# Performance work log

Hardware: AMD Instinct MI355X
Metric: run time of the kernel (lower is better)

The kernel has to match this reference:

```python
import jax, jax.numpy as jnp
import numpy as np

SPARSITY_RATIO = 0.1


def setup_inputs() -> dict:
    key = jax.random.key(0)
    ks = jax.random.split(key, 11)
    B, S, d = 4, 2048, 16  # d = n_sparse_dims + 2
    inp = {
        "full": jax.random.normal(ks[0], (B, S, d), dtype=jnp.float32),
        "sw1": jax.random.normal(ks[1], (d, 32), dtype=jnp.float32) * 0.1,
        "sb1": jax.random.normal(ks[2], (32,), dtype=jnp.float32) * 0.1,
        "sw2": jax.random.normal(ks[3], (32, 1), dtype=jnp.float32) * 0.1,
        "sb2": jax.random.normal(ks[4], (1,), dtype=jnp.float32) * 0.1,
        "mw1": jax.random.normal(ks[5], (3 * d, 64), dtype=jnp.float32) * 0.1,
        "mb1": jax.random.normal(ks[6], (64,), dtype=jnp.float32) * 0.1,
        "mw2": jax.random.normal(ks[7], (64, 32), dtype=jnp.float32) * 0.1,
        "mb2": jax.random.normal(ks[8], (32,), dtype=jnp.float32) * 0.1,
        "mw3": jax.random.normal(ks[9], (32, d), dtype=jnp.float32) * 0.1,
        "mb3": jax.random.normal(ks[10], (d,), dtype=jnp.float32) * 0.1,
    }
    return inp


def reference(full, sw1, sb1, sw2, sb2, mw1, mb1, mw2, mb2, mw3, mb3):
    B, S, d = full.shape
    k = max(1, int(S * SPARSITY_RATIO))  # static python int

    # importance scores: Linear(d,32) -> ReLU -> Linear(32,1)
    scores = (jax.nn.relu(full @ sw1 + sb1) @ sw2 + sb2)[..., 0]  # [B, S]
    _, top_idx = jax.lax.top_k(scores, k)  # [B, k]

    # gather selected tokens (keys == values)
    sel = jnp.take_along_axis(full, top_idx[:, :, None], axis=1)  # [B, k, d]

    # First MLP layer on concat([q, keys, values]) decomposed to avoid the
    # [B,S,k,3d] concat: mw1 splits into query / key / value blocks.
    w_q, w_k, w_v = mw1[:d], mw1[d:2 * d], mw1[2 * d:]
    q_part = full @ w_q                     # [B, S, 64]
    kv_part = sel @ (w_k + w_v)             # [B, k, 64]
    h1 = jax.nn.relu(q_part[:, :, None, :] + kv_part[:, None, :, :] + mb1)  # [B,S,k,64]
    h2 = jax.nn.relu(h1 @ mw2 + mb2)        # [B, S, k, 32]
    out = h2 @ mw3 + mb3                    # [B, S, k, d]
    return out.mean(axis=2)                 # [B, S, d]
```

## Files before the change

kernel.cpp:

```cpp
#include <hip/hip_runtime.h>
#include <hip/hip_bf16.h>

#define BB 4
#define SS 2048
#define DD 16
#define KK 204
#define JSPLIT 8

typedef __attribute__((ext_vector_type(8))) short short8;
typedef __attribute__((ext_vector_type(4))) float f32x4;

__device__ inline short f2bf(float x) {
  __hip_bfloat16 b = __float2bfloat16(x);
  return *reinterpret_cast<short*>(&b);
}

__global__ void __launch_bounds__(256) score_q_kernel(
    const float* __restrict__ full, const float* __restrict__ sw1,
    const float* __restrict__ sb1, const float* __restrict__ sw2,
    const float* __restrict__ sb2, const float* __restrict__ mw1,
    float* __restrict__ scores, float* __restrict__ qpart) {
  int idx = blockIdx.x * blockDim.x + threadIdx.x;
  if (idx >= BB * SS) return;
  float x[16];
  const float* xp = full + idx * DD;
#pragma unroll
  for (int i = 0; i < 16; i++) x[i] = xp[i];

  float sc = sb2[0];
#pragma unroll
  for (int n = 0; n < 32; n++) {
    float a = sb1[n];
#pragma unroll
    for (int k = 0; k < 16; k++) a += x[k] * sw1[k * 32 + n];
    a = fmaxf(a, 0.f);
    sc += a * sw2[n];
  }
  scores[idx] = sc;

#pragma unroll
  for (int n = 0; n < 64; n++) {
    float a = 0.f;
#pragma unroll
    for (int k = 0; k < 16; k++) a += x[k] * mw1[k * 64 + n];
    qpart[idx * 64 + n] = a;
  }
}

__global__ void __launch_bounds__(256) topk_kvb_kernel(
    const float* __restrict__ scores, const float* __restrict__ full,
    const float* __restrict__ mw1, const float* __restrict__ mb1,
    float* __restrict__ kvb) {
  int b = blockIdx.x;
  int t = threadIdx.x;
  int lane = t & 63, w = t >> 6;

  __shared__ int hist[2048];
  __shared__ int wtot[4];
  __shared__ unsigned long long s_pfx;
  __shared__ int s_r;
  __shared__ int s_idx[KK];
  __shared__ float s_x[KK * DD];

  float wreg[16];
#pragma unroll
  for (int k = 0; k < 16; k++)
    wreg[k] = mw1[(16 + k) * 64 + lane] + mw1[(32 + k) * 64 + lane];
  float biasv = mb1[lane];

  unsigned long long key[8];
#pragma unroll
  for (int e = 0; e < 8; e++) {
    int i = t + e * 256;
    float f = scores[b * SS + i];
    unsigned u = __float_as_uint(f);
    u = (u & 0x80000000u) ? ~u : (u | 0x80000000u);
    key[e] = ((unsigned long long)u << 11) | (unsigned)(SS - 1 - i);
  }
  if (t == 0) { s_pfx = 0ull; s_r = KK; }

#pragma unroll
  for (int pass = 0; pass < 4; pass++) {
    int s = 33 - pass * 11;
#pragma unroll
    for (int z = 0; z < 8; z++) hist[t + z * 256] = 0;
    __syncthreads();
    unsigned long long pfx = s_pfx;
    int r = s_r;
#pragma unroll
    for (int e = 0; e < 8; e++) {
      if ((key[e] >> (s + 11)) == pfx)
        atomicAdd(&hist[(int)((key[e] >> s) & 0x7FF)], 1);
    }
    __syncthreads();
    int loc[8], ls[9];
#pragma unroll
    for (int i = 0; i < 8; i++) loc[i] = hist[t * 8 + i];
    ls[8] = 0;
#pragma unroll
    for (int i = 7; i >= 0; i--) ls[i] = ls[i + 1] + loc[i];
    int tot = ls[0];
    int incl = tot;
#pragma unroll
    for (int off = 1; off < 64; off <<= 1) {
      int o = __shfl_down(incl, off);
      incl += (lane + off < 64) ? o : 0;
    }
    if (lane == 0) wtot[w] = incl;
    __syncthreads();
    int waveoff = 0;
    for (int ww = w + 1; ww < 4; ww++) waveoff += wtot[ww];
    int excl_thread = waveoff + (incl - tot);
#pragma unroll
    for (int i = 0; i < 8; i++) {
      int sufs = ls[i] + excl_thread;
      int sufn = ls[i + 1] + excl_thread;
      if (sufs >= r && sufn < r) {
        s_pfx = (pfx << 11) | (unsigned)(t * 8 + i);
        s_r = r - sufn;
      }
    }
    __syncthreads();
  }

  unsigned long long kstar = s_pfx;
  bool selm[8];
  int c = 0;
#pragma unroll
  for (int e = 0; e < 8; e++) {
    selm[e] = (key[e] >= kstar);
    c += selm[e] ? 1 : 0;
  }
  int p = c;
#pragma unroll
  for (int off = 1; off < 64; off <<= 1) {
    int o = __shfl_up(p, off);
    p += (lane >= off) ? o : 0;
  }
  if (lane == 63) wtot[w] = p;
  __syncthreads();
  int base = 0;
  for (int ww = 0; ww < w; ww++) base += wtot[ww];
  int pos = base + p - c;
#pragma unroll
  for (int e = 0; e < 8; e++) {
    if (selm[e]) s_idx[pos++] = t + e * 256;
  }
  __syncthreads();

  for (int i = t; i < KK * DD; i += 256) {
    int j = i >> 4, e = i & 15;
    s_x[i] = full[(b * SS + s_idx[j]) * DD + e];
  }
  __syncthreads();

  for (int j = w; j < KK; j += 4) {
    const float* xr = &s_x[j * DD];
    float a = biasv;
#pragma unroll
    for (int k = 0; k < 16; k++) a += xr[k] * wreg[k];
    kvb[(b * KK + j) * 64 + lane] = a;
  }
}

__global__ void __launch_bounds__(512) main_mfma_kernel(
    const float* __restrict__ qpart, const float* __restrict__ kvb,
    const float* __restrict__ mw2, const float* __restrict__ mb2,
    const float* __restrict__ mw3, const float* __restrict__ mb3,
    float* __restrict__ out) {
  int mtile = blockIdx.x;
  int bs_base = mtile * 16;
  int b = bs_base >> 11;
  int t = threadIdx.x;
  int w = t >> 6;
  int l = t & 63;
  int ml = l & 15;
  int g = l >> 4;

  __shared__ float s_kvb[KK * 64];
  float (*red)[512] = (float(*)[512])s_kvb;

  {
    const f32x4* src = (const f32x4*)(kvb + b * KK * 64);
    f32x4* dst = (f32x4*)s_kvb;
    for (int i = t; i < KK * 16; i += 512) dst[i] = src[i];
  }

  f32x4 qv[2][2];
  {
    const float* qp = qpart + (bs_base + ml) * 64 + 8 * g;
    qv[0][0] = *(const f32x4*)(qp);
    qv[0][1] = *(const f32x4*)(qp + 4);
    qv[1][0] = *(const f32x4*)(qp + 32);
    qv[1][1] = *(const f32x4*)(qp + 36);
  }

  short8 bfrag[2][2];
#pragma unroll
  for (int nt = 0; nt < 2; nt++)
#pragma unroll
    for (int kh = 0; kh < 2; kh++)
#pragma unroll
      for (int i = 0; i < 8; i++) {
        int k = kh * 32 + 8 * g + i;
        bfrag[nt][kh][i] = f2bf(mw2[k * 32 + nt * 16 + ml]);
      }

  f32x4 biasfrag[2];
#pragma unroll
  for (int nt = 0; nt < 2; nt++) {
    float bv = mb2[nt * 16 + ml];
    f32x4 bf;
    bf[0] = bv; bf[1] = bv; bf[2] = bv; bf[3] = bv;
    biasfrag[nt] = bf;
  }

  float accs[2][4] = {};
  int jbeg = w * 26;
  int jend = jbeg + 26;
  if (jend > KK) jend = KK;

  __syncthreads();

  const float* kvbl = s_kvb + 8 * g;
#pragma unroll 2
  for (int j = jbeg; j < jend; j++) {
    const float* kp = kvbl + j * 64;
    f32x4 kv[2][2];
    kv[0][0] = *(const f32x4*)(kp);
    kv[0][1] = *(const f32x4*)(kp + 4);
    kv[1][0] = *(const f32x4*)(kp + 32);
    kv[1][1] = *(const f32x4*)(kp + 36);

    short8 afrag[2];
#pragma unroll
    for (int kh = 0; kh < 2; kh++)
#pragma unroll
      for (int hf = 0; hf < 2; hf++)
#pragma unroll
        for (int i = 0; i < 4; i++) {
          float h = fmaxf(qv[kh][hf][i] + kv[kh][hf][i], 0.f);
          afrag[kh][hf * 4 + i] = f2bf(h);
        }

#pragma unroll
    for (int nt = 0; nt < 2; nt++) {
      f32x4 c = __builtin_amdgcn_mfma_f32_16x16x32_bf16(
          afrag[0], bfrag[nt][0], biasfrag[nt], 0, 0, 0);
      c = __builtin_amdgcn_mfma_f32_16x16x32_bf16(
          afrag[1], bfrag[nt][1], c, 0, 0, 0);
#pragma unroll
      for (int r = 0; r < 4; r++) accs[nt][r] += fmaxf(c[r], 0.f);
    }
  }

  __syncthreads();
#pragma unroll
  for (int nt = 0; nt < 2; nt++)
#pragma unroll
    for (int r = 0; r < 4; r++)
      red[w][(4 * g + r) * 32 + nt * 16 + ml] = accs[nt][r];
  __syncthreads();
  float sum = 0.f;
#pragma unroll
  for (int ww = 0; ww < JSPLIT; ww++) sum += red[ww][t];
  sum *= (1.0f / (float)KK);
  red[0][t] = sum;
  __syncthreads();

  if (t < 256) {
    int m = t >> 4, dc = t & 15;
    float o = mb3[dc];
#pragma unroll
    for (int n = 0; n < 32; n++) o += red[0][m * 32 + n] * mw3[n * 16 + dc];
    out[(bs_base + m) * 16 + dc] = o;
  }
}

extern "C" void kernel_launch(void* const* d_in, const int* in_sizes, int n_in,
                              void* d_out, int out_size, void* d_ws, size_t ws_size,
                              hipStream_t stream) {
  const float* full = (const float*)d_in[0];
  const float* sw1  = (const float*)d_in[1];
  const float* sb1  = (const float*)d_in[2];
  const float* sw2  = (const float*)d_in[3];
  const float* sb2  = (const float*)d_in[4];
  const float* mw1  = (const float*)d_in[5];
  const float* mb1  = (const float*)d_in[6];
  const float* mw2  = (const float*)d_in[7];
  const float* mb2  = (const float*)d_in[8];
  const float* mw3  = (const float*)d_in[9];
  const float* mb3  = (const float*)d_in[10];
  float* out = (float*)d_out;

  float* ws = (float*)d_ws;
  float* scores = ws;
  float* qpart  = scores + BB * SS;
  float* kvb    = qpart + BB * SS * 64;

  score_q_kernel<<<(BB * SS) / 256, 256, 0, stream>>>(full, sw1, sb1, sw2, sb2,
                                                      mw1, scores, qpart);
  topk_kvb_kernel<<<BB, 256, 0, stream>>>(scores, full, mw1, mb1, kvb);
  main_mfma_kernel<<<BB * SS / 16, 512, 0, stream>>>(qpart, kvb, mw2, mb2, mw3,
                                                     mb3, out);
}
```

Before: 44.70 us.

## Fuse scoring into top-k kernel and compute query projection inside main kernel

Removes the separate score/qpart kernel. Scores are now computed inside the per-batch top-k kernel, which grows to 512 threads. The query projection is recomputed per tile in shared memory inside the main MFMA kernel. This drops one launch and the 2 MB qpart write and read, but the scoring MLP now runs on only 4 blocks, serialising 2048 tokens' worth of work per block.

Result: slower. 93.45 us (+109.1%).

```diff
diff --git a/kernel.cpp b/kernel.cpp
--- a/kernel.cpp
+++ b/kernel.cpp
@@ -15,108 +15,79 @@
   return *reinterpret_cast<short*>(&b);
 }
 
-__global__ void __launch_bounds__(256) score_q_kernel(
+__global__ void __launch_bounds__(512) topk_kvb_kernel(
     const float* __restrict__ full, const float* __restrict__ sw1,
     const float* __restrict__ sb1, const float* __restrict__ sw2,
     const float* __restrict__ sb2, const float* __restrict__ mw1,
-    float* __restrict__ scores, float* __restrict__ qpart) {
-  int idx = blockIdx.x * blockDim.x + threadIdx.x;
-  if (idx >= BB * SS) return;
-  float x[16];
-  const float* xp = full + idx * DD;
-#pragma unroll
-  for (int i = 0; i < 16; i++) x[i] = xp[i];
-
-  float sc = sb2[0];
-#pragma unroll
-  for (int n = 0; n < 32; n++) {
-    float a = sb1[n];
-#pragma unroll
-    for (int k = 0; k < 16; k++) a += x[k] * sw1[k * 32 + n];
-    a = fmaxf(a, 0.f);
-    sc += a * sw2[n];
-  }
-  scores[idx] = sc;
-
-#pragma unroll
-  for (int n = 0; n < 64; n++) {
-    float a = 0.f;
-#pragma unroll
-    for (int k = 0; k < 16; k++) a += x[k] * mw1[k * 64 + n];
-    qpart[idx * 64 + n] = a;
-  }
-}
-
-__global__ void __launch_bounds__(256) topk_kvb_kernel(
-    const float* __restrict__ scores, const float* __restrict__ full,
-    const float* __restrict__ mw1, const float* __restrict__ mb1,
-    float* __restrict__ kvb) {
+    const float* __restrict__ mb1, float* __restrict__ kvb_g) {
   int b = blockIdx.x;
   int t = threadIdx.x;
-  int lane = t & 63, w = t >> 6;
+  int l = t & 63, w = t >> 6;
 
   __shared__ int hist[2048];
-  __shared__ int wtot[4];
+  __shared__ float s_x[KK * DD];
+  __shared__ int s_idx[KK];
+  __shared__ int wtot[8];
   __shared__ unsigned long long s_pfx;
   __shared__ int s_r;
-  __shared__ int s_idx[KK];
-  __shared__ float s_x[KK * DD];
-
-  float wreg[16];
-#pragma unroll
-  for (int k = 0; k < 16; k++)
-    wreg[k] = mw1[(16 + k) * 64 + lane] + mw1[(32 + k) * 64 + lane];
-  float biasv = mb1[lane];
-
-  unsigned long long key[8];
-#pragma unroll
-  for (int e = 0; e < 8; e++) {
-    int i = t + e * 256;
-    float f = scores[b * SS + i];
-    unsigned u = __float_as_uint(f);
+
+  unsigned long long key[4];
+#pragma unroll
+  for (int e = 0; e < 4; e++) {
+    int i = t + e * 512;
+    const float* xp = full + (b * SS + i) * DD;
+    float x[16];
+#pragma unroll
+    for (int k = 0; k < 16; k++) x[k] = xp[k];
+    float sc = sb2[0];
+#pragma unroll
+    for (int n = 0; n < 32; n++) {
+      float a = sb1[n];
+#pragma unroll
+      for (int k = 0; k < 16; k++) a += x[k] * sw1[k * 32 + n];
+      sc += fmaxf(a, 0.f) * sw2[n];
+    }
+    unsigned u = __float_as_uint(sc);
     u = (u & 0x80000000u) ? ~u : (u | 0x80000000u);
     key[e] = ((unsigned long long)u << 11) | (unsigned)(SS - 1 - i);
   }
   if (t == 0) { s_pfx = 0ull; s_r = KK; }
 
-#pragma unroll
   for (int pass = 0; pass < 4; pass++) {
     int s = 33 - pass * 11;
 #pragma unroll
-    for (int z = 0; z < 8; z++) hist[t + z * 256] = 0;
+    for (int z = 0; z < 4; z++) hist[t * 4 + z] = 0;
     __syncthreads();
     unsigned long long pfx = s_pfx;
     int r = s_r;
 #pragma unroll
-    for (int e = 0; e < 8; e++) {
+    for (int e = 0; e < 4; e++)
       if ((key[e] >> (s + 11)) == pfx)
         atomicAdd(&hist[(int)((key[e] >> s) & 0x7FF)], 1);
-    }
-    __syncthreads();
-    int loc[8], ls[9];
-#pragma unroll
-    for (int i = 0; i < 8; i++) loc[i] = hist[t * 8 + i];
-    ls[8] = 0;
-#pragma unroll
-    for (int i = 7; i >= 0; i--) ls[i] = ls[i + 1] + loc[i];
+    __syncthreads();
+    int loc[4], ls[5];
+#pragma unroll
+    for (int i2 = 0; i2 < 4; i2++) loc[i2] = hist[t * 4 + i2];
+    ls[4] = 0;
+#pragma unroll
+    for (int i2 = 3; i2 >= 0; i2--) ls[i2] = ls[i2 + 1] + loc[i2];
     int tot = ls[0];
     int incl = tot;
 #pragma unroll
     for (int off = 1; off < 64; off <<= 1) {
       int o = __shfl_down(incl, off);
-      incl += (lane + off < 64) ? o : 0;
-    }
-    if (lane == 0) wtot[w] = incl;
+      incl += (l + off < 64) ? o : 0;
+    }
+    if (l == 0) wtot[w] = incl;
     __syncthreads();
     int waveoff = 0;
-    for (int ww = w + 1; ww < 4; ww++) waveoff += wtot[ww];
-    int excl_thread = waveoff + (incl - tot);
-#pragma unroll
-    for (int i = 0; i < 8; i++) {
-      int sufs = ls[i] + excl_thread;
-      int sufn = ls[i + 1] + excl_thread;
+    for (int ww = w + 1; ww < 8; ww++) waveoff += wtot[ww];
+    int excl = waveoff + (incl - tot);
+#pragma unroll
+    for (int i2 = 0; i2 < 4; i2++) {
+      int sufs = ls[i2] + excl, sufn = ls[i2 + 1] + excl;
       if (sufs >= r && sufn < r) {
-        s_pfx = (pfx << 11) | (unsigned)(t * 8 + i);
+        s_pfx = (pfx << 11) | (unsigned)(t * 4 + i2);
         s_r = r - sufn;
       }
     }
@@ -124,10 +95,10 @@
   }
 
   unsigned long long kstar = s_pfx;
-  bool selm[8];
+  bool selm[4];
   int c = 0;
 #pragma unroll
-  for (int e = 0; e < 8; e++) {
+  for (int e = 0; e < 4; e++) {
     selm[e] = (key[e] >= kstar);
     c += selm[e] ? 1 : 0;
   }
@@ -135,39 +106,40 @@
 #pragma unroll
   for (int off = 1; off < 64; off <<= 1) {
     int o = __shfl_up(p, off);
-    p += (lane >= off) ? o : 0;
-  }
-  if (lane == 63) wtot[w] = p;
+    p += (l >= off) ? o : 0;
+  }
+  if (l == 63) wtot[w] = p;
   __syncthreads();
   int base = 0;
   for (int ww = 0; ww < w; ww++) base += wtot[ww];
   int pos = base + p - c;
 #pragma unroll
-  for (int e = 0; e < 8; e++) {
-    if (selm[e]) s_idx[pos++] = t + e * 256;
-  }
-  __syncthreads();
-
-  for (int i = t; i < KK * DD; i += 256) {
-    int j = i >> 4, e = i & 15;
-    s_x[i] = full[(b * SS + s_idx[j]) * DD + e];
-  }
-  __syncthreads();
-
-  for (int j = w; j < KK; j += 4) {
-    const float* xr = &s_x[j * DD];
+  for (int e = 0; e < 4; e++)
+    if (selm[e]) s_idx[pos++] = t + e * 512;
+  __syncthreads();
+
+  for (int i = t; i < KK * DD; i += 512)
+    s_x[i] = full[(b * SS + s_idx[i >> 4]) * DD + (i & 15)];
+  float wreg[16];
+#pragma unroll
+  for (int k = 0; k < 16; k++)
+    wreg[k] = mw1[(16 + k) * 64 + l] + mw1[(32 + k) * 64 + l];
+  float biasv = mb1[l];
+  __syncthreads();
+  for (int j = w; j < KK; j += 8) {
+    const float* xr = s_x + j * DD;
     float a = biasv;
 #pragma unroll
     for (int k = 0; k < 16; k++) a += xr[k] * wreg[k];
-    kvb[(b * KK + j) * 64 + lane] = a;
+    kvb_g[(b * KK + j) * 64 + l] = a;
   }
 }
 
 __global__ void __launch_bounds__(512) main_mfma_kernel(
-    const float* __restrict__ qpart, const float* __restrict__ kvb,
+    const float* __restrict__ full, const float* __restrict__ mw1,
     const float* __restrict__ mw2, const float* __restrict__ mb2,
     const float* __restrict__ mw3, const float* __restrict__ mb3,
-    float* __restrict__ out) {
+    const float* __restrict__ kvb_g, float* __restrict__ out) {
   int mtile = blockIdx.x;
   int bs_base = mtile * 16;
   int b = bs_base >> 11;
@@ -178,21 +150,29 @@
   int g = l >> 4;
 
   __shared__ float s_kvb[KK * 64];
+  __shared__ float qs[16 * 64];
+  __shared__ float xs[16 * 16];
   float (*red)[512] = (float(*)[512])s_kvb;
 
   {
-    const f32x4* src = (const f32x4*)(kvb + b * KK * 64);
+    const f32x4* src = (const f32x4*)(kvb_g + b * KK * 64);
     f32x4* dst = (f32x4*)s_kvb;
     for (int i = t; i < KK * 16; i += 512) dst[i] = src[i];
   }
-
-  f32x4 qv[2][2];
+  if (t < 256) xs[t] = full[bs_base * DD + t];
+  __syncthreads();
+
   {
-    const float* qp = qpart + (bs_base + ml) * 64 + 8 * g;
-    qv[0][0] = *(const f32x4*)(qp);
-    qv[0][1] = *(const f32x4*)(qp + 4);
-    qv[1][0] = *(const f32x4*)(qp + 32);
-    qv[1][1] = *(const f32x4*)(qp + 36);
+    int r = t >> 5, n = t & 31;
+    float q0 = 0.f, q1 = 0.f;
+#pragma unroll
+    for (int k = 0; k < 16; k++) {
+      float xv = xs[r * 16 + k];
+      q0 += xv * mw1[k * 64 + n];
+      q1 += xv * mw1[k * 64 + n + 32];
+    }
+    qs[r * 64 + n] = q0;
+    qs[r * 64 + n + 32] = q1;
   }
 
   short8 bfrag[2][2];
@@ -205,7 +185,6 @@
         int k = kh * 32 + 8 * g + i;
         bfrag[nt][kh][i] = f2bf(mw2[k * 32 + nt * 16 + ml]);
       }
-
   f32x4 biasfrag[2];
 #pragma unroll
   for (int nt = 0; nt < 2; nt++) {
@@ -214,14 +193,21 @@
     bf[0] = bv; bf[1] = bv; bf[2] = bv; bf[3] = bv;
     biasfrag[nt] = bf;
   }
+  __syncthreads();
+
+  f32x4 qv[2][2];
+  {
+    const float* qp = qs + ml * 64 + 8 * g;
+    qv[0][0] = *(const f32x4*)(qp);
+    qv[0][1] = *(const f32x4*)(qp + 4);
+    qv[1][0] = *(const f32x4*)(qp + 32);
+    qv[1][1] = *(const f32x4*)(qp + 36);
+  }
 
   float accs[2][4] = {};
   int jbeg = w * 26;
   int jend = jbeg + 26;
   if (jend > KK) jend = KK;
-
-  __syncthreads();
-
   const float* kvbl = s_kvb + 8 * g;
 #pragma unroll 2
   for (int j = jbeg; j < jend; j++) {
@@ -293,14 +279,10 @@
   const float* mb3  = (const float*)d_in[10];
   float* out = (float*)d_out;
 
-  float* ws = (float*)d_ws;
-  float* scores = ws;
-  float* qpart  = scores + BB * SS;
-  float* kvb    = qpart + BB * SS * 64;
-
-  score_q_kernel<<<(BB * SS) / 256, 256, 0, stream>>>(full, sw1, sb1, sw2, sb2,
-                                                      mw1, scores, qpart);
-  topk_kvb_kernel<<<BB, 256, 0, stream>>>(scores, full, mw1, mb1, kvb);
-  main_mfma_kernel<<<BB * SS / 16, 512, 0, stream>>>(qpart, kvb, mw2, mb2, mw3,
-                                                     mb3, out);
-}
+  float* kvb_g = (float*)d_ws;
+
+  topk_kvb_kernel<<<BB, 512, 0, stream>>>(full, sw1, sb1, sw2, sb2, mw1, mb1,
+                                          kvb_g);
+  main_mfma_kernel<<<BB * SS / 16, 512, 0, stream>>>(full, mw1, mw2, mb2, mw3,
+                                                     mb3, kvb_g, out);
+}
```
